# Kernel tuning notes

Measured on AMD Instinct MI355X. Metric: run time of the kernel, lower is better.

The kernel has to match this reference:

```python
import jax, jax.numpy as jnp
import numpy as np

N, E, D_IN, HID, D_OUT = 200000, 5000000, 128, 16, 2


def setup_inputs() -> dict:
    key = jax.random.key(0)
    ks = jax.random.split(key, 8)
    x = jax.random.normal(ks[0], (N, D_IN), dtype=jnp.float32)
    edge_index = jax.random.randint(ks[1], (2, E), 0, N, dtype=jnp.int32)
    W1 = jax.random.normal(ks[2], (D_IN, HID), dtype=jnp.float32) / np.sqrt(D_IN)
    b1 = jnp.zeros((HID,), dtype=jnp.float32)
    W3 = jax.random.normal(ks[3], (HID, HID), dtype=jnp.float32) / np.sqrt(HID)
    b3 = jnp.zeros((HID,), dtype=jnp.float32)
    W2 = jax.random.normal(ks[4], (HID, D_OUT), dtype=jnp.float32) / np.sqrt(HID)
    b2 = jnp.zeros((D_OUT,), dtype=jnp.float32)
    return {"x": x, "edge_index": edge_index, "W1": W1, "b1": b1,
            "W3": W3, "b3": b3, "W2": W2, "b2": b2}


def reference(x, edge_index, W1, b1, W3, b3, W2, b2):
    # GCNConv: add self-loops, symmetric normalization, aggregate, linear+bias.
    src, dst = edge_index[0], edge_index[1]
    loops = jnp.arange(N, dtype=src.dtype)
    src_f = jnp.concatenate([src, loops])  # [E+N]
    dst_f = jnp.concatenate([dst, loops])
    deg = jax.ops.segment_sum(jnp.ones_like(src_f, dtype=jnp.float32), dst_f,
                              num_segments=N)
    dis = jnp.where(deg > 0, jax.lax.rsqrt(jnp.maximum(deg, 1.0)), 0.0)
    norm = dis[src_f] * dis[dst_f]  # [E+N]

    def gcn_conv(h, W, b):
        h = h @ W                                   # [N, F_out] small GEMM
        msg = h[src_f] * norm[:, None]              # gather + scale
        agg = jax.ops.segment_sum(msg, dst_f, num_segments=N)  # scatter-add
        return agg + b

    h = jax.nn.relu(gcn_conv(x, W1, b1))    # conv1 (dropout is identity in eval)
    h = jax.nn.relu(gcn_conv(h, W3, b3))    # conv3 loop (conv_number-2 = 1 iter)
    h = gcn_conv(h, W2, b2)                 # conv2
    return jax.nn.log_softmax(h, axis=1)
```

## Files before the change

kernel.cpp:

```cpp
#include <hip/hip_runtime.h>

#define NN 200000
#define NE 5000000
#define DIN 128
#define HID 16
#define DOUT 2
#define BSZ 391
#define NB 512
#define LBITS 9
#define NCH 8
#define SLICE_DIV 25000
#define NK (NB * NCH)
#define PB 256
#define PT 512
#define CAP 2048

static_assert((size_t)NB * BSZ >= NN, "bucket coverage");
static_assert((NN - 1) / SLICE_DIV == NCH - 1, "slice count");


__global__ __launch_bounds__(PT) void hist_pass(const int* __restrict__ src,
                                                const int* __restrict__ dst,
                                                int* __restrict__ blockHist) {
    __shared__ int h[NK];
    for (int k = threadIdx.x; k < NK; k += PT) h[k] = 0;
    __syncthreads();
    for (int i = blockIdx.x * PT + threadIdx.x; i < NE; i += PB * PT) {
        int dv = dst[i];
        int sv = src[i];
        atomicAdd(&h[((dv / BSZ) << 3) + sv / SLICE_DIV], 1);
    }
    __syncthreads();
    for (int k = threadIdx.x; k < NK; k += PT)
        blockHist[(size_t)blockIdx.x * NK + k] = h[k];
}

__global__ __launch_bounds__(256) void tot_pass(const int* __restrict__ blockHist,
                                                int* __restrict__ chunkStart) {
    int k = blockIdx.x * 256 + threadIdx.x;
    if (k >= NK) return;
    int s = 0;
#pragma unroll 8
    for (int b = 0; b < PB; ++b) s += blockHist[(size_t)b * NK + k];
    chunkStart[k] = s;
}

__global__ __launch_bounds__(1024) void scan_keys(int* __restrict__ chunkStart) {
    __shared__ int psum[1024];
    int t = threadIdx.x;
    const int KPT = (NK + 1023) / 1024;
    int k0 = t * KPT; if (k0 > NK) k0 = NK;
    int k1 = k0 + KPT; if (k1 > NK) k1 = NK;
    int vals[KPT];
    int s = 0;
    for (int k = k0; k < k1; ++k) { vals[k - k0] = chunkStart[k]; s += vals[k - k0]; }
    psum[t] = s;
    __syncthreads();
    for (int off = 1; off < 1024; off <<= 1) {
        int add = (t >= off) ? psum[t - off] : 0;
        __syncthreads();
        psum[t] += add;
        __syncthreads();
    }
    int run = psum[t] - s;
    for (int k = k0; k < k1; ++k) { chunkStart[k] = run; run += vals[k - k0]; }
    if (t == 0) chunkStart[NK] = NE;
}

__global__ __launch_bounds__(256) void offsets_pass(int* __restrict__ blockHist,
                                                    const int* __restrict__ chunkStart) {
    int k = blockIdx.x * 256 + threadIdx.x;
    if (k >= NK) return;
    int r = chunkStart[k];
#pragma unroll 8
    for (int b = 0; b < PB; ++b) {
        size_t idx = (size_t)b * NK + k;
        int v = blockHist[idx];
        blockHist[idx] = r;
        r += v;
    }
}

__global__ __launch_bounds__(PT) void scatter_pass(const int* __restrict__ src,
                                                   const int* __restrict__ dst,
                                                   const int* __restrict__ blockHist,
                                                   unsigned* __restrict__ pedge) {
    __shared__ int cur[NK];
    for (int k = threadIdx.x; k < NK; k += PT)
        cur[k] = blockHist[(size_t)blockIdx.x * NK + k];
    __syncthreads();
    for (int i = blockIdx.x * PT + threadIdx.x; i < NE; i += PB * PT) {
        int sv = src[i];
        int dv = dst[i];
        int bk = dv / BSZ;
        int key = (bk << 3) + sv / SLICE_DIV;
        int pos = atomicAdd(&cur[key], 1);
        pedge[pos] = ((unsigned)sv << LBITS) | (unsigned)(dv - bk * BSZ);
    }
}


__global__ __launch_bounds__(512) void subsort(const unsigned* __restrict__ pedge,
                                               const int* __restrict__ chunkStart,
                                               int* __restrict__ pedge2,
                                               int* __restrict__ rowStart,
                                               float* __restrict__ dis) {
    __shared__ unsigned ebuf[CAP];
    __shared__ int hist[512];
    __shared__ int cur[512];
    __shared__ int wsum[8];
    int t = threadIdx.x;
    int b = blockIdx.x;
    int lane = t & 63, w = t >> 6;
    int deg = 1;
    const unsigned LM = (1u << LBITS) - 1u;
    for (int s = 0; s < NCH; ++s) {
        int seg = b * NCH + s;
        int e0 = chunkStart[seg], e1 = chunkStart[seg + 1];
        int n = e1 - e0;
        hist[t] = 0;
        __syncthreads();
        for (int i = t; i < n; i += 512) {
            unsigned p = pedge[e0 + i];
            ebuf[i] = p;
            atomicAdd(&hist[p & LM], 1);
        }
        __syncthreads();
        int v = hist[t];
        deg += v;
        int inc = v;
        for (int off = 1; off < 64; off <<= 1) {
            int nb = __shfl_up(inc, off, 64);
            if (lane >= off) inc += nb;
        }
        if (lane == 63) wsum[w] = inc;
        __syncthreads();
        if (t == 0) {
            int car = 0;
#pragma unroll
            for (int i = 0; i < 8; ++i) { int u = wsum[i]; wsum[i] = car; car += u; }
        }
        __syncthreads();
        int excl = inc - v + wsum[w];
        if (t < BSZ) rowStart[(size_t)seg * BSZ + t] = e0 + excl;
        cur[t] = excl;
        __syncthreads();
        for (int i = t; i < n; i += 512) {
            unsigned p = ebuf[i];
            int pos = atomicAdd(&cur[p & LM], 1);
            pedge2[e0 + pos] = (int)(p >> LBITS);
        }
        __syncthreads();
    }
    int node = b * BSZ + t;
    if (t < BSZ && node < NN) dis[node] = rsqrtf((float)deg);
    if (b == 0 && t == 0) rowStart[(size_t)NK * BSZ] = NE;
}


#define GXR 64
#define XPAD 132
__global__ __launch_bounds__(256) void gemm_x_w1(const float* __restrict__ x,
                                                 const float* __restrict__ W,
                                                 const float* __restrict__ dis,
                                                 float* __restrict__ out) {
    __shared__ float w[DIN * HID];
    __shared__ float xt[GXR * XPAD];
    int t = threadIdx.x;
    for (int i = t; i < DIN * HID; i += 256) w[i] = W[i];
    int rbase = blockIdx.x * GXR;
    const float4* xg = reinterpret_cast<const float4*>(x + (size_t)rbase * DIN);
    float4* xt4 = reinterpret_cast<float4*>(xt);
    for (int i = t; i < GXR * (DIN / 4); i += 256) {
        int row = i >> 5, kk = i & 31;
        xt4[row * (XPAD / 4) + kk] = xg[i];
    }
    __syncthreads();
    int row = t >> 2;
    int c0 = (t & 3) * 4;
    const float* xr = xt + row * XPAD;
    float ax = 0.f, ay = 0.f, az = 0.f, aw = 0.f;
#pragma unroll 4
    for (int k = 0; k < DIN; ++k) {
        float xv = xr[k];
        float4 wv = *reinterpret_cast<const float4*>(&w[k * HID + c0]);
        ax += xv * wv.x; ay += xv * wv.y; az += xv * wv.z; aw += xv * wv.w;
    }
    int node = rbase + row;
    float dd = dis[node];
    *reinterpret_cast<float4*>(&out[(size_t)node * HID + c0]) =
        make_float4(ax * dd, ay * dd, az * dd, aw * dd);
}

__global__ __launch_bounds__(256) void gemm_h_w16(const float* __restrict__ h,
                                                  const float* __restrict__ W,
                                                  const float* __restrict__ dis,
                                                  float* __restrict__ out) {
    __shared__ float w[HID * HID];
    if (threadIdx.x < HID * HID) w[threadIdx.x] = W[threadIdx.x];
    __syncthreads();
    int row = blockIdx.x * 16 + (threadIdx.x >> 4);
    int c = threadIdx.x & 15;
    if (row >= NN) return;
    const float4* hr = reinterpret_cast<const float4*>(h + (size_t)row * HID);
    float acc = 0.f;
#pragma unroll
    for (int k4 = 0; k4 < HID / 4; ++k4) {
        float4 v = hr[k4];
        acc += v.x * w[(4 * k4 + 0) * HID + c] + v.y * w[(4 * k4 + 1) * HID + c]
             + v.z * w[(4 * k4 + 2) * HID + c] + v.w * w[(4 * k4 + 3) * HID + c];
    }
    out[row * HID + c] = acc * dis[row];
}

__global__ __launch_bounds__(256) void gemm_h_w2(const float* __restrict__ h,
                                                 const float* __restrict__ W,
                                                 const float* __restrict__ dis,
                                                 float* __restrict__ out) {
    int t = blockIdx.x * 256 + threadIdx.x;
    int row = t >> 1;
    int c = t & 1;
    if (row >= NN) return;
    const float* hr = h + (size_t)row * HID;
    float acc = 0.f;
#pragma unroll
    for (int k = 0; k < HID; ++k) acc += hr[k] * W[k * DOUT + c];
    out[row * DOUT + c] = acc * dis[row];
}


__device__ __forceinline__ void acc_edges(const int* __restrict__ pedge2,
                                          const float4* __restrict__ xs4,
                                          int e, int e1, int c4, float4& a) {
    for (; e + 3 < e1; e += 4) {
        int s0 = pedge2[e], s1 = pedge2[e + 1];
        int s2 = pedge2[e + 2], s3 = pedge2[e + 3];
        float4 u0 = xs4[(s0 << 2) + c4];
        float4 u1 = xs4[(s1 << 2) + c4];
        float4 u2 = xs4[(s2 << 2) + c4];
        float4 u3 = xs4[(s3 << 2) + c4];
        a.x += (u0.x + u1.x) + (u2.x + u3.x);
        a.y += (u0.y + u1.y) + (u2.y + u3.y);
        a.z += (u0.z + u1.z) + (u2.z + u3.z);
        a.w += (u0.w + u1.w) + (u2.w + u3.w);
    }
    for (; e < e1; ++e) {
        float4 u = xs4[(pedge2[e] << 2) + c4];
        a.x += u.x; a.y += u.y; a.z += u.z; a.w += u.w;
    }
}

__global__ __launch_bounds__(1024, 8) void agg16_all(const int* __restrict__ pedge2,
                                                     const int* __restrict__ rowStart,
                                                     const float* __restrict__ xs,
                                                     const float* __restrict__ dis,
                                                     const float* __restrict__ bias,
                                                     float* __restrict__ buf,
                                                     int relu) {
    int t = threadIdx.x;
    int b = blockIdx.x;
    int base = b * BSZ;
    int c4 = t & 3;
    int q = t >> 2;
    int g0 = (q * BSZ) >> 8;
    int g1 = ((q + 1) * BSZ) >> 8;
    bool two = (g1 - g0) == 2;
    int n0 = base + g0, n1 = base + g0 + 1;
    bool v0 = n0 < NN;
    bool v1 = two && (n1 < NN);
    const float4* xs4 = reinterpret_cast<const float4*>(xs);
    float4* buf4 = reinterpret_cast<float4*>(buf);
    float4 a0 = make_float4(0.f, 0.f, 0.f, 0.f);
    float4 a1 = a0;
    if (v0) a0 = xs4[(n0 << 2) + c4];
    if (v1) a1 = xs4[(n1 << 2) + c4];
    for (int r = 0; r < NCH; ++r) {
        const int* rs = rowStart + (size_t)(b * NCH + r) * BSZ;
        if (v0) acc_edges(pedge2, xs4, rs[g0], rs[g0 + 1], c4, a0);
        if (v1) acc_edges(pedge2, xs4, rs[g0 + 1], rs[g0 + 2], c4, a1);
    }
    float4 bb = reinterpret_cast<const float4*>(bias)[c4];
    if (v0) {
        float dd = dis[n0];
        float4 v = make_float4(dd * a0.x + bb.x, dd * a0.y + bb.y,
                               dd * a0.z + bb.z, dd * a0.w + bb.w);
        if (relu) { v.x = fmaxf(v.x, 0.f); v.y = fmaxf(v.y, 0.f);
                    v.z = fmaxf(v.z, 0.f); v.w = fmaxf(v.w, 0.f); }
        buf4[(n0 << 2) + c4] = v;
    }
    if (v1) {
        float dd = dis[n1];
        float4 v = make_float4(dd * a1.x + bb.x, dd * a1.y + bb.y,
                               dd * a1.z + bb.z, dd * a1.w + bb.w);
        if (relu) { v.x = fmaxf(v.x, 0.f); v.y = fmaxf(v.y, 0.f);
                    v.z = fmaxf(v.z, 0.f); v.w = fmaxf(v.w, 0.f); }
        buf4[(n1 << 2) + c4] = v;
    }
}

__global__ __launch_bounds__(512) void agg2_lsm(const int* __restrict__ pedge2,
                                                const int* __restrict__ rowStart,
                                                const float* __restrict__ xs,
                                                const float* __restrict__ dis,
                                                const float* __restrict__ bias,
                                                float* __restrict__ out) {
    int t = threadIdx.x;
    int b = blockIdx.x;
    if (t >= BSZ) return;
    int node = b * BSZ + t;
    if (node >= NN) return;
    const float2* xs2 = reinterpret_cast<const float2*>(xs);
    float a0 = 0.f, a1 = 0.f;
    for (int s = 0; s < NCH; ++s) {
        const int* rs = rowStart + (size_t)(b * NCH + s) * BSZ;
        int e = rs[t], e1 = rs[t + 1];
        for (; e + 3 < e1; e += 4) {
            int s0 = pedge2[e], s1 = pedge2[e + 1];
            int s2 = pedge2[e + 2], s3 = pedge2[e + 3];
            float2 v0 = xs2[s0], v1 = xs2[s1], v2 = xs2[s2], v3 = xs2[s3];
            a0 += (v0.x + v1.x) + (v2.x + v3.x);
            a1 += (v0.y + v1.y) + (v2.y + v3.y);
        }
        for (; e < e1; ++e) {
            float2 v = xs2[pedge2[e]];
            a0 += v.x; a1 += v.y;
        }
    }
    float2 sv = xs2[node];
    float d = dis[node];
    float v0 = (a0 + sv.x) * d + bias[0];
    float v1 = (a1 + sv.y) * d + bias[1];
    float m = fmaxf(v0, v1);
    float lse = m + logf(__expf(v0 - m) + __expf(v1 - m));
    reinterpret_cast<float2*>(out)[node] = make_float2(v0 - lse, v1 - lse);
}


extern "C" void kernel_launch(void* const* d_in, const int* in_sizes, int n_in,
                              void* d_out, int out_size, void* d_ws, size_t ws_size,
                              hipStream_t stream) {
    const float* x = (const float*)d_in[0];
    const int* ei = (const int*)d_in[1];
    const float* W1 = (const float*)d_in[2];
    const float* b1 = (const float*)d_in[3];
    const float* W3 = (const float*)d_in[4];
    const float* b3 = (const float*)d_in[5];
    const float* W2 = (const float*)d_in[6];
    const float* b2 = (const float*)d_in[7];
    float* out = (float*)d_out;

    const int* src = ei;
    const int* dst = ei + NE;

    int* W = (int*)d_ws;
    unsigned* pedge = (unsigned*)W;
    int* pedge2 = W + NE;
    int* rowStart = W + 2 * (size_t)NE;
    int* blockHist = rowStart + (size_t)NK * BSZ + 4;
    int* chunkStart = blockHist + (size_t)PB * NK;
    float* dis = (float*)(chunkStart + NK + 4);
    float* bufB = dis + NN;
    float* bufA = (float*)W;

    const int B = 256;
    auto cdiv = [](long long a, long long b) { return (int)((a + b - 1) / b); };

    hist_pass<<<PB, PT, 0, stream>>>(src, dst, blockHist);
    tot_pass<<<cdiv(NK, 256), 256, 0, stream>>>(blockHist, chunkStart);
    scan_keys<<<1, 1024, 0, stream>>>(chunkStart);
    offsets_pass<<<cdiv(NK, 256), 256, 0, stream>>>(blockHist, chunkStart);
    scatter_pass<<<PB, PT, 0, stream>>>(src, dst, blockHist, pedge);
    subsort<<<NB, 512, 0, stream>>>(pedge, chunkStart, pedge2, rowStart, dis);

    gemm_x_w1<<<NN / GXR, B, 0, stream>>>(x, W1, dis, bufA);
    agg16_all<<<NB, 1024, 0, stream>>>(pedge2, rowStart, bufA, dis, b1, bufB, 1);

    gemm_h_w16<<<cdiv(NN, 16), B, 0, stream>>>(bufB, W3, dis, bufA);
    agg16_all<<<NB, 1024, 0, stream>>>(pedge2, rowStart, bufA, dis, b3, bufB, 1);

    gemm_h_w2<<<cdiv((long long)NN * DOUT, B), B, 0, stream>>>(bufB, W2, dis, bufA);
    agg2_lsm<<<NB, 512, 0, stream>>>(pedge2, rowStart, bufA, dis, b2, out);
}
```

Baseline: 318.4 us.

## Partition edges by destination bucket only, sub-sort by slice in subsort

The global counting-sort pass now keys only on the 512 destination buckets instead of 4096 (bucket, source-slice) keys. The slice-major ordering is produced inside subsort with a 4096-entry shared histogram over the whole bucket. This shrinks the per-block histograms, the scan and the offsets passes, and drops the source read in hist_pass. In exchange, subsort reads each bucket's edges from global memory twice instead of caching them in LDS, and the larger shared histogram may lower occupancy.

```diff
diff --git a/kernel.cpp b/kernel.cpp
--- a/kernel.cpp
+++ b/kernel.cpp
@@ -11,70 +11,67 @@
 #define NCH 8
 #define SLICE_DIV 25000
 #define NK (NB * NCH)
+#define NKB 512
+#define SKEYS 4096
 #define PB 256
 #define PT 512
-#define CAP 2048
 
 static_assert((size_t)NB * BSZ >= NN, "bucket coverage");
 static_assert((NN - 1) / SLICE_DIV == NCH - 1, "slice count");
 
 
-__global__ __launch_bounds__(PT) void hist_pass(const int* __restrict__ src,
-                                                const int* __restrict__ dst,
+__global__ __launch_bounds__(PT) void hist_pass(const int* __restrict__ dst,
                                                 int* __restrict__ blockHist) {
-    __shared__ int h[NK];
-    for (int k = threadIdx.x; k < NK; k += PT) h[k] = 0;
-    __syncthreads();
-    for (int i = blockIdx.x * PT + threadIdx.x; i < NE; i += PB * PT) {
-        int dv = dst[i];
-        int sv = src[i];
-        atomicAdd(&h[((dv / BSZ) << 3) + sv / SLICE_DIV], 1);
-    }
-    __syncthreads();
-    for (int k = threadIdx.x; k < NK; k += PT)
-        blockHist[(size_t)blockIdx.x * NK + k] = h[k];
+    __shared__ int h[NKB];
+    for (int k = threadIdx.x; k < NKB; k += PT) h[k] = 0;
+    __syncthreads();
+    for (int i = blockIdx.x * PT + threadIdx.x; i < NE; i += PB * PT)
+        atomicAdd(&h[dst[i] / BSZ], 1);
+    __syncthreads();
+    for (int k = threadIdx.x; k < NKB; k += PT)
+        blockHist[(size_t)blockIdx.x * NKB + k] = h[k];
 }
 
 __global__ __launch_bounds__(256) void tot_pass(const int* __restrict__ blockHist,
                                                 int* __restrict__ chunkStart) {
     int k = blockIdx.x * 256 + threadIdx.x;
-    if (k >= NK) return;
+    if (k >= NKB) return;
     int s = 0;
 #pragma unroll 8
-    for (int b = 0; b < PB; ++b) s += blockHist[(size_t)b * NK + k];
+    for (int b = 0; b < PB; ++b) s += blockHist[(size_t)b * NKB + k];
     chunkStart[k] = s;
 }
 
-__global__ __launch_bounds__(1024) void scan_keys(int* __restrict__ chunkStart) {
-    __shared__ int psum[1024];
-    int t = threadIdx.x;
-    const int KPT = (NK + 1023) / 1024;
-    int k0 = t * KPT; if (k0 > NK) k0 = NK;
-    int k1 = k0 + KPT; if (k1 > NK) k1 = NK;
-    int vals[KPT];
-    int s = 0;
-    for (int k = k0; k < k1; ++k) { vals[k - k0] = chunkStart[k]; s += vals[k - k0]; }
-    psum[t] = s;
-    __syncthreads();
-    for (int off = 1; off < 1024; off <<= 1) {
-        int add = (t >= off) ? psum[t - off] : 0;
-        __syncthreads();
-        psum[t] += add;
-        __syncthreads();
-    }
-    int run = psum[t] - s;
-    for (int k = k0; k < k1; ++k) { chunkStart[k] = run; run += vals[k - k0]; }
-    if (t == 0) chunkStart[NK] = NE;
+__global__ __launch_bounds__(NKB) void scan_keys(int* __restrict__ chunkStart) {
+    __shared__ int wsum[8];
+    int t = threadIdx.x;
+    int lane = t & 63, w = t >> 6;
+    int v = chunkStart[t];
+    int inc = v;
+    for (int off = 1; off < 64; off <<= 1) {
+        int nb = __shfl_up(inc, off, 64);
+        if (lane >= off) inc += nb;
+    }
+    if (lane == 63) wsum[w] = inc;
+    __syncthreads();
+    if (t == 0) {
+        int car = 0;
+#pragma unroll
+        for (int i = 0; i < 8; ++i) { int u = wsum[i]; wsum[i] = car; car += u; }
+    }
+    __syncthreads();
+    chunkStart[t] = inc - v + wsum[w];
+    if (t == 0) chunkStart[NKB] = NE;
 }
 
 __global__ __launch_bounds__(256) void offsets_pass(int* __restrict__ blockHist,
                                                     const int* __restrict__ chunkStart) {
     int k = blockIdx.x * 256 + threadIdx.x;
-    if (k >= NK) return;
+    if (k >= NKB) return;
     int r = chunkStart[k];
 #pragma unroll 8
     for (int b = 0; b < PB; ++b) {
-        size_t idx = (size_t)b * NK + k;
+        size_t idx = (size_t)b * NKB + k;
         int v = blockHist[idx];
         blockHist[idx] = r;
         r += v;
@@ -85,16 +82,15 @@
                                                    const int* __restrict__ dst,
                                                    const int* __restrict__ blockHist,
                                                    unsigned* __restrict__ pedge) {
-    __shared__ int cur[NK];
-    for (int k = threadIdx.x; k < NK; k += PT)
-        cur[k] = blockHist[(size_t)blockIdx.x * NK + k];
+    __shared__ int cur[NKB];
+    for (int k = threadIdx.x; k < NKB; k += PT)
+        cur[k] = blockHist[(size_t)blockIdx.x * NKB + k];
     __syncthreads();
     for (int i = blockIdx.x * PT + threadIdx.x; i < NE; i += PB * PT) {
         int sv = src[i];
         int dv = dst[i];
         int bk = dv / BSZ;
-        int key = (bk << 3) + sv / SLICE_DIV;
-        int pos = atomicAdd(&cur[key], 1);
+        int pos = atomicAdd(&cur[bk], 1);
         pedge[pos] = ((unsigned)sv << LBITS) | (unsigned)(dv - bk * BSZ);
     }
 }
@@ -105,55 +101,62 @@
                                                int* __restrict__ pedge2,
                                                int* __restrict__ rowStart,
                                                float* __restrict__ dis) {
-    __shared__ unsigned ebuf[CAP];
-    __shared__ int hist[512];
-    __shared__ int cur[512];
+    __shared__ int h[SKEYS];
     __shared__ int wsum[8];
     int t = threadIdx.x;
     int b = blockIdx.x;
     int lane = t & 63, w = t >> 6;
-    int deg = 1;
-    const unsigned LM = (1u << LBITS) - 1u;
-    for (int s = 0; s < NCH; ++s) {
-        int seg = b * NCH + s;
-        int e0 = chunkStart[seg], e1 = chunkStart[seg + 1];
-        int n = e1 - e0;
-        hist[t] = 0;
-        __syncthreads();
-        for (int i = t; i < n; i += 512) {
-            unsigned p = pedge[e0 + i];
-            ebuf[i] = p;
-            atomicAdd(&hist[p & LM], 1);
-        }
-        __syncthreads();
-        int v = hist[t];
-        deg += v;
-        int inc = v;
-        for (int off = 1; off < 64; off <<= 1) {
-            int nb = __shfl_up(inc, off, 64);
-            if (lane >= off) inc += nb;
-        }
-        if (lane == 63) wsum[w] = inc;
-        __syncthreads();
-        if (t == 0) {
-            int car = 0;
-#pragma unroll
-            for (int i = 0; i < 8; ++i) { int u = wsum[i]; wsum[i] = car; car += u; }
-        }
-        __syncthreads();
-        int excl = inc - v + wsum[w];
-        if (t < BSZ) rowStart[(size_t)seg * BSZ + t] = e0 + excl;
-        cur[t] = excl;
-        __syncthreads();
-        for (int i = t; i < n; i += 512) {
-            unsigned p = ebuf[i];
-            int pos = atomicAdd(&cur[p & LM], 1);
-            pedge2[e0 + pos] = (int)(p >> LBITS);
-        }
-        __syncthreads();
-    }
-    int node = b * BSZ + t;
-    if (t < BSZ && node < NN) dis[node] = rsqrtf((float)deg);
+    int e0 = chunkStart[b], e1 = chunkStart[b + 1];
+    for (int k = t; k < SKEYS; k += 512) h[k] = 0;
+    __syncthreads();
+    for (int i = e0 + t; i < e1; i += 512) {
+        unsigned p = pedge[i];
+        int sv = (int)(p >> LBITS);
+        atomicAdd(&h[(sv / SLICE_DIV) * 512 + (p & 511u)], 1);
+    }
+    __syncthreads();
+    if (t < BSZ) {
+        int dg = 1;
+#pragma unroll
+        for (int s = 0; s < NCH; ++s) dg += h[s * 512 + t];
+        int node = b * BSZ + t;
+        if (node < NN) dis[node] = rsqrtf((float)dg);
+    }
+    int vals[8];
+    int s = 0;
+#pragma unroll
+    for (int j = 0; j < 8; ++j) { vals[j] = h[t * 8 + j]; s += vals[j]; }
+    int inc = s;
+    for (int off = 1; off < 64; off <<= 1) {
+        int nb = __shfl_up(inc, off, 64);
+        if (lane >= off) inc += nb;
+    }
+    if (lane == 63) wsum[w] = inc;
+    __syncthreads();
+    if (t == 0) {
+        int car = 0;
+#pragma unroll
+        for (int i = 0; i < 8; ++i) { int u = wsum[i]; wsum[i] = car; car += u; }
+    }
+    __syncthreads();
+    int run = inc - s + wsum[w];
+#pragma unroll
+    for (int j = 0; j < 8; ++j) {
+        int k = t * 8 + j;
+        h[k] = run;
+        int dl = k & 511, sl = k >> 9;
+        if (dl < BSZ)
+            rowStart[(size_t)(b * NCH + sl) * BSZ + dl] = e0 + run;
+        run += vals[j];
+    }
+    __syncthreads();
+    for (int i = e0 + t; i < e1; i += 512) {
+        unsigned p = pedge[i];
+        int sv = (int)(p >> LBITS);
+        int key = (sv / SLICE_DIV) * 512 + (p & 511u);
+        int pos = atomicAdd(&h[key], 1);
+        pedge2[e0 + pos] = sv;
+    }
     if (b == 0 && t == 0) rowStart[(size_t)NK * BSZ] = NE;
 }
 
@@ -357,18 +360,18 @@
     int* pedge2 = W + NE;
     int* rowStart = W + 2 * (size_t)NE;
     int* blockHist = rowStart + (size_t)NK * BSZ + 4;
-    int* chunkStart = blockHist + (size_t)PB * NK;
-    float* dis = (float*)(chunkStart + NK + 4);
+    int* chunkStart = blockHist + (size_t)PB * NKB;
+    float* dis = (float*)(chunkStart + NKB + 4);
     float* bufB = dis + NN;
     float* bufA = (float*)W;
 
     const int B = 256;
     auto cdiv = [](long long a, long long b) { return (int)((a + b - 1) / b); };
 
-    hist_pass<<<PB, PT, 0, stream>>>(src, dst, blockHist);
-    tot_pass<<<cdiv(NK, 256), 256, 0, stream>>>(blockHist, chunkStart);
-    scan_keys<<<1, 1024, 0, stream>>>(chunkStart);
-    offsets_pass<<<cdiv(NK, 256), 256, 0, stream>>>(blockHist, chunkStart);
+    hist_pass<<<PB, PT, 0, stream>>>(dst, blockHist);
+    tot_pass<<<cdiv(NKB, 256), 256, 0, stream>>>(blockHist, chunkStart);
+    scan_keys<<<1, NKB, 0, stream>>>(chunkStart);
+    offsets_pass<<<cdiv(NKB, 256), 256, 0, stream>>>(blockHist, chunkStart);
     scatter_pass<<<PB, PT, 0, stream>>>(src, dst, blockHist, pedge);
     subsort<<<NB, 512, 0, stream>>>(pedge, chunkStart, pedge2, rowStart, dis);
 
```

Measured after the change: 305.6 us. 4.0% less time.
